# Kernel tuning notes

Measured on AMD Instinct MI355X. Metric: run time of the kernel, lower is better.

The kernel has to match this reference:

```python
import jax, jax.numpy as jnp
import numpy as np

B, T, S = 2, 1024, 2048            # batch, query len, cache size
D, N, KH, H = 4096, 32, 8, 128     # emb_dim, q heads, kv heads, head_dim
ROPE_THETA = 1000000
EPS = 1e-6
K_MASK = jnp.finfo(jnp.bfloat16).min


def _rms_norm(x, scale):
    dtype = x.dtype
    rms = jnp.sqrt(jnp.mean(x.astype(jnp.float32) ** 2, axis=-1, keepdims=True) + EPS)
    return (scale * x / rms).astype(dtype)


def _rope_sincos(positions, head_dim):
    fraction = jnp.arange(0, head_dim, 2, dtype=jnp.float32) / head_dim
    inv_freq = 1.0 / (ROPE_THETA ** fraction)
    sinusoid = jnp.einsum('BT,k->BTk', positions.astype(jnp.float32), inv_freq,
                          precision=jax.lax.Precision.HIGHEST)
    return jnp.sin(sinusoid), jnp.cos(sinusoid)


def _apply_rope(x, sin, cos):
    half = x.shape[-1] // 2
    x1, x2 = x[..., :half], x[..., half:]
    sin, cos = sin[:, :, None, :], cos[:, :, None, :]
    return jnp.concatenate([x1 * cos - x2 * sin, x2 * cos + x1 * sin], axis=-1).astype(x.dtype)


def setup_inputs() -> dict:
    key = jax.random.key(0)
    ks = jax.random.split(key, 8)
    std = 0.01  # nnx.initializers.normal() default stddev
    return {
        'x': jax.random.normal(ks[0], (B, T, D), dtype=jnp.float32),
        'wq': jax.random.normal(ks[1], (D, N, H), dtype=jnp.float32) * std,
        'wk': jax.random.normal(ks[2], (D, KH, H), dtype=jnp.float32) * std,
        'wv': jax.random.normal(ks[3], (D, KH, H), dtype=jnp.float32) * std,
        'wo': jax.random.normal(ks[4], (N, H, D), dtype=jnp.float32) * std,
        'q_scale': jnp.ones((H,), dtype=jnp.float32),
        'k_scale': jnp.ones((H,), dtype=jnp.float32),
        'k_cache': jnp.zeros((B, S, KH, H), dtype=jnp.float32),
        'v_cache': jnp.zeros((B, S, KH, H), dtype=jnp.float32),
        'segment_ids': jnp.ones((B, T), dtype=jnp.int32),
        'num_right_pads': 0,
    }


def reference(x, wq, wk, wv, wo, q_scale, k_scale, k_cache, v_cache, segment_ids, num_right_pads):
    b, t, _ = x.shape
    s = k_cache.shape[1]
    n, kh, h = wq.shape[1], wk.shape[1], wq.shape[2]
    cur_ind = 0  # empty cache (prefill)

    q = _rms_norm(jnp.einsum('BTD,DNH->BTNH', x, wq), q_scale)      # [B,T,N,H]
    key = _rms_norm(jnp.einsum('BSD,DKH->BSKH', x, wk), k_scale)    # [B,T,K,H]
    val = jnp.einsum('BSD,DKH->BSKH', x, wv)                         # [B,T,K,H]

    # start_ind < 0 initially -> count left pads from segment_ids
    start = jnp.sum(jnp.cumsum(segment_ids != 0, axis=-1) == 0, -1).astype(jnp.int32)
    first = jnp.argmax(segment_ids, axis=1)
    pos = jnp.where(segment_ids != 0, jnp.arange(t, dtype=jnp.int32) - first[:, None], 2 ** 30)
    position_ids = pos + cur_ind

    sin, cos = _rope_sincos(position_ids, h)
    q = _apply_rope(q, sin, cos)
    key = _apply_rope(key, sin, cos)

    k_cache = jax.lax.dynamic_update_slice(k_cache, key, (0, cur_ind, 0, 0))
    v_cache = jax.lax.dynamic_update_slice(v_cache, val, (0, cur_ind, 0, 0))

    g = n // kh
    qr = q.reshape(b, t, kh, g, h)
    logits = jnp.einsum('BTHGD,BSHD->BHGTS', qr, k_cache) * (h ** -0.5)

    q_pos = cur_ind + jnp.arange(t, dtype=jnp.int32)[None, :] - start[:, None]
    ts = jnp.arange(s, dtype=jnp.int32)
    kv_seg = ((ts[None, :] >= start[:, None]) & (ts[None, :] < cur_ind + t)).astype(segment_ids.dtype)
    k_pos = ts[None, :] - start[:, None]
    causal = k_pos[:, None, :] <= q_pos[:, :, None]                  # [B,T,S]
    seg_mask = kv_seg[:, None, :] == segment_ids[:, :, None]        # [B,T,S]
    mask = causal & seg_mask

    logits = jnp.where(mask[:, None, None, :, :], logits, K_MASK)
    w = jax.nn.softmax(logits.astype(jnp.float32), axis=-1).astype(logits.dtype)
    qkv = jnp.einsum('BHGTS,BSHD->BTHGD', w, v_cache).reshape(b, t, n, h)
    return jnp.einsum('BTNH,NHD->BTD', qkv, wo)
```

## Files before the change

kernel.cpp:

```cpp
#include <hip/hip_runtime.h>

constexpr int Bc  = 2;
constexpr int Tc  = 1024;
constexpr int Dc  = 4096;
constexpr int NHc = 32;
constexpr int KHc = 8;
constexpr int Hc  = 128;

typedef __bf16 bf16;
typedef bf16  bf16x4  __attribute__((ext_vector_type(4)));
typedef bf16  bf16x8  __attribute__((ext_vector_type(8)));
typedef float floatx4 __attribute__((ext_vector_type(4)));

#define MFMA16(a, b, c) __builtin_amdgcn_mfma_f32_16x16x32_bf16((a), (b), (c), 0, 0, 0)

__device__ __forceinline__ void gload_lds16(const bf16* g, bf16* l) {
    __builtin_amdgcn_global_load_lds(
        (const __attribute__((address_space(1))) void*)g,
        (__attribute__((address_space(3))) void*)l, 16, 0, 0);
}

__global__ void seg_scan(const int* __restrict__ seg, int* __restrict__ start) {
    int b = threadIdx.x;
    if (b >= Bc) return;
    int f = 0;
    for (int t = 0; t < Tc; ++t) {
        if (seg[b * Tc + t] != 0) { f = t; break; }
    }
    start[b] = f;
}

__global__ __launch_bounds__(256) void cvt_f32_bf16(const float* __restrict__ in,
                                                    bf16* __restrict__ out) {
    const size_t i = ((size_t)blockIdx.x * 256 + threadIdx.x) * 8;
    float4 f0 = *(const float4*)(in + i);
    float4 f1 = *(const float4*)(in + i + 4);
    bf16x8 v;
    v[0] = (bf16)f0.x; v[1] = (bf16)f0.y; v[2] = (bf16)f0.z; v[3] = (bf16)f0.w;
    v[4] = (bf16)f1.x; v[5] = (bf16)f1.y; v[6] = (bf16)f1.z; v[7] = (bf16)f1.w;
    *(bf16x8*)(out + i) = v;
}

__global__ __launch_bounds__(256) void transpose_cvt(const float* __restrict__ in,
                                                     bf16* __restrict__ out,
                                                     int R, int C) {
    __shared__ float tile[64][65];
    const int c0 = blockIdx.x * 64, r0 = blockIdx.y * 64;
    const int tx = threadIdx.x & 15, ty = threadIdx.x >> 4;
#pragma unroll
    for (int i = 0; i < 4; ++i) {
        float4 f = *(const float4*)&in[(size_t)(r0 + ty * 4 + i) * C + c0 + tx * 4];
        tile[ty * 4 + i][tx * 4 + 0] = f.x;
        tile[ty * 4 + i][tx * 4 + 1] = f.y;
        tile[ty * 4 + i][tx * 4 + 2] = f.z;
        tile[ty * 4 + i][tx * 4 + 3] = f.w;
    }
    __syncthreads();
#pragma unroll
    for (int i = 0; i < 4; ++i) {
        const int cc = ty * 4 + i;
        bf16x4 v;
        v[0] = (bf16)tile[tx * 4 + 0][cc];
        v[1] = (bf16)tile[tx * 4 + 1][cc];
        v[2] = (bf16)tile[tx * 4 + 2][cc];
        v[3] = (bf16)tile[tx * 4 + 3][cc];
        *(bf16x4*)&out[(size_t)(c0 + cc) * R + r0 + tx * 4] = v;
    }
}

__global__ __launch_bounds__(256) void v_transpose(const bf16* __restrict__ src,
                                                   bf16* __restrict__ dst,
                                                   int srcstride) {
    __shared__ bf16 tl[32][136];
    const int bk = blockIdx.y;
    const int b = bk / KHc, kh = bk % KHc;
    const int t0 = blockIdx.x * 32;
    const int tid = threadIdx.x;
    {
        const int j = tid >> 3;
        const int c = tid & 7;
        const bf16* p = src + (size_t)(b * Tc + t0 + j) * srcstride + kh * Hc + c * 16;
        *(bf16x8*)&tl[j][c * 16]     = *(const bf16x8*)p;
        *(bf16x8*)&tl[j][c * 16 + 8] = *(const bf16x8*)(p + 8);
    }
    __syncthreads();
    {
        const int d = tid >> 1;
        const int toff = (tid & 1) * 16;
        bf16x8 v0, v1;
#pragma unroll
        for (int k = 0; k < 8; ++k) v0[k] = tl[toff + k][d];
#pragma unroll
        for (int k = 0; k < 8; ++k) v1[k] = tl[toff + 8 + k][d];
        bf16* o = dst + ((size_t)bk * Hc + d) * Tc + t0 + toff;
        *(bf16x8*)o       = v0;
        *(bf16x8*)(o + 8) = v1;
    }
}

template <typename OT>
__global__ __launch_bounds__(256) void gemm128(const bf16* __restrict__ A,
                                               const bf16* __restrict__ Bt,
                                               OT* __restrict__ C,
                                               int M, int K, int N) {
    __shared__ alignas(16) bf16 As[128 * 32];
    __shared__ alignas(16) bf16 Bs[128 * 32];
    const int m0 = blockIdx.y * 128, n0 = blockIdx.x * 128;
    const int tid = threadIdx.x;
    const int w = tid >> 6, L = tid & 63, quad = L >> 4, lid = L & 15;
    const int wm = (w & 1) * 64, wn = (w >> 1) * 64;

    const int srow = w * 32 + (L >> 2);
    const int chk  = (L & 3) ^ ((L >> 3) & 3);
    const bf16* gA = A  + (size_t)(m0 + srow) * K + chk * 8;
    const bf16* gB = Bt + (size_t)(n0 + srow) * K + chk * 8;
    bf16* lA0 = &As[(w * 32) * 32];
    bf16* lA1 = &As[(w * 32 + 16) * 32];
    bf16* lB0 = &Bs[(w * 32) * 32];
    bf16* lB1 = &Bs[(w * 32 + 16) * 32];

    const bf16* ap[4]; const bf16* bp[4];
#pragma unroll
    for (int i = 0; i < 4; ++i) {
        const int ra = wm + i * 16 + lid;
        ap[i] = &As[ra * 32 + (quad ^ ((ra >> 1) & 3)) * 8];
        const int rb = wn + i * 16 + lid;
        bp[i] = &Bs[rb * 32 + (quad ^ ((rb >> 1) & 3)) * 8];
    }

    floatx4 acc[4][4] = {};

    for (int k0 = 0; k0 < K; k0 += 32) {
        __syncthreads();
        gload_lds16(gA + k0,                  lA0);
        gload_lds16(gA + (size_t)16 * K + k0, lA1);
        gload_lds16(gB + k0,                  lB0);
        gload_lds16(gB + (size_t)16 * K + k0, lB1);
        __syncthreads();

        bf16x8 af[4], bfr[4];
#pragma unroll
        for (int i = 0; i < 4; ++i) af[i]  = *(const bf16x8*)ap[i];
#pragma unroll
        for (int j = 0; j < 4; ++j) bfr[j] = *(const bf16x8*)bp[j];
#pragma unroll
        for (int i = 0; i < 4; ++i)
#pragma unroll
            for (int j = 0; j < 4; ++j)
                acc[i][j] = MFMA16(af[i], bfr[j], acc[i][j]);
    }

#pragma unroll
    for (int i = 0; i < 4; ++i) {
#pragma unroll
        for (int r = 0; r < 4; ++r) {
            const size_t row = (size_t)(m0 + wm + i * 16 + quad * 4 + r);
#pragma unroll
            for (int j = 0; j < 4; ++j)
                C[row * N + (n0 + wn + j * 16 + lid)] = (OT)acc[i][j][r];
        }
    }
}

template <typename OT>
__global__ __launch_bounds__(512, 2) void gemm_ring256(const bf16* __restrict__ A,
                                                       const bf16* __restrict__ Bt,
                                                       OT* __restrict__ C,
                                                       int M, int K, int N) {
    __shared__ alignas(16) bf16 ring[4][16384];
    const int m0 = blockIdx.y * 256, n0 = blockIdx.x * 256;
    const int tid = threadIdx.x;
    const int w = tid >> 6, L = tid & 63, quad = L >> 4, lid = L & 15;
    const int wr = w >> 2, wc = w & 3;

    const int srow = tid >> 2;
    const int schk = ((tid & 3) ^ ((tid >> 3) & 3)) * 8;
    const bf16* gA0 = A  + (size_t)(m0 + srow) * K + schk;
    const bf16* gA1 = A  + (size_t)(m0 + 128 + srow) * K + schk;
    const bf16* gB0 = Bt + (size_t)(n0 + srow) * K + schk;
    const bf16* gB1 = Bt + (size_t)(n0 + 128 + srow) * K + schk;
    const int ldsA0 = (w * 16) * 32;
    const int ldsA1 = (128 + w * 16) * 32;
    const int ldsB0 = 8192 + (w * 16) * 32;
    const int ldsB1 = 8192 + (128 + w * 16) * 32;

    int offA[8], offB[4];
#pragma unroll
    for (int m = 0; m < 8; ++m) {
        const int row = wr * 128 + m * 16 + lid;
        offA[m] = row * 32 + ((quad ^ ((row >> 1) & 3)) * 8);
    }
#pragma unroll
    for (int n = 0; n < 4; ++n) {
        const int row = wc * 64 + n * 16 + lid;
        offB[n] = 8192 + row * 32 + ((quad ^ ((row >> 1) & 3)) * 8);
    }

    const int NT = K >> 5;

    auto stage = [&](int kt) {
        bf16* sb = ring[kt & 3];
        const size_t ko = (size_t)kt << 5;
        gload_lds16(gA0 + ko, sb + ldsA0);
        gload_lds16(gA1 + ko, sb + ldsA1);
        gload_lds16(gB0 + ko, sb + ldsB0);
        gload_lds16(gB1 + ko, sb + ldsB1);
    };

    stage(0); stage(1); stage(2);
    asm volatile("s_waitcnt vmcnt(8)" ::: "memory");
    __builtin_amdgcn_s_barrier();
    __builtin_amdgcn_sched_barrier(0);

    floatx4 acc[8][4] = {};

    for (int t = 0; t < NT; ++t) {
        int ts = t + 3; if (ts >= NT) ts -= NT;
        stage(ts);

        const bf16* sb = ring[t & 3];
        bf16x8 af[8], bfr[4];
#pragma unroll
        for (int m = 0; m < 8; ++m) af[m]  = *(const bf16x8*)(sb + offA[m]);
#pragma unroll
        for (int n = 0; n < 4; ++n) bfr[n] = *(const bf16x8*)(sb + offB[n]);

        __builtin_amdgcn_s_setprio(1);
#pragma unroll
        for (int m = 0; m < 8; ++m)
#pragma unroll
            for (int n = 0; n < 4; ++n)
                acc[m][n] = MFMA16(af[m], bfr[n], acc[m][n]);
        __builtin_amdgcn_s_setprio(0);

        asm volatile("s_waitcnt vmcnt(8)" ::: "memory");
        __builtin_amdgcn_s_barrier();
        __builtin_amdgcn_sched_barrier(0);
    }

    asm volatile("s_waitcnt vmcnt(0)" ::: "memory");

#pragma unroll
    for (int m = 0; m < 8; ++m) {
#pragma unroll
        for (int r = 0; r < 4; ++r) {
            const size_t row = (size_t)(m0 + wr * 128 + m * 16 + quad * 4 + r);
#pragma unroll
            for (int n = 0; n < 4; ++n)
                C[row * N + (n0 + wc * 64 + n * 16 + lid)] = (OT)acc[m][n][r];
        }
    }
}

__global__ __launch_bounds__(256) void rms_rope(bf16* __restrict__ buf,
                                                const float* __restrict__ scale,
                                                const int* __restrict__ start,
                                                int nheads, int rowstride) {
    const int gid = blockIdx.x * 4 + (threadIdx.x >> 6);
    const int L   = threadIdx.x & 63;
    const int h   = gid % nheads;
    const int t   = (gid / nheads) % Tc;
    const int b   = gid / (nheads * Tc);
    bf16* p = buf + (size_t)(b * Tc + t) * rowstride + h * Hc;

    float x1 = (float)p[L], x2 = (float)p[L + 64];
    float ss = x1 * x1 + x2 * x2;
#pragma unroll
    for (int off = 1; off < 64; off <<= 1) ss += __shfl_xor(ss, off);
    const float inv = 1.f / sqrtf(ss * (1.0f / 128.0f) + 1e-6f);
    const float y1 = scale[L] * x1 * inv;
    const float y2 = scale[L + 64] * x2 * inv;

    const int   pos = t - start[b];
    const float fr  = (float)L * (1.0f / 64.0f);
    const float invf = exp2f(-19.9315686f * fr);
    const float ang = (float)pos * invf;
    float sn, cs;
    sincosf(ang, &sn, &cs);

    p[L]      = (bf16)(y1 * cs - y2 * sn);
    p[L + 64] = (bf16)(y2 * cs + y1 * sn);
}

__global__ __launch_bounds__(256) void attn_kernel(const bf16* __restrict__ q,
                                                   const bf16* __restrict__ k,
                                                   const bf16* __restrict__ vt,
                                                   bf16* __restrict__ outp,
                                                   const int* __restrict__ start,
                                                   int qstride, int kstride) {
    __shared__ alignas(16) bf16 Ks[32 * 128];
    __shared__ alignas(16) bf16 VT[128 * 32];
    __shared__ alignas(16) bf16 pS[4][16][40];

    const int tblk = blockIdx.x, n = blockIdx.y, b = blockIdx.z;
    const int kh   = n >> 2;
    const int tid  = threadIdx.x, w = tid >> 6, L = tid & 63;
    const int quad = L >> 4, lid = L & 15;
    const int t0   = tblk * 64 + w * 16;
    const int st   = start[b];

    const bf16* qrow = q + (size_t)(b * Tc + t0 + lid) * qstride + n * Hc;
    bf16x8 aqf[4];
#pragma unroll
    for (int c = 0; c < 4; ++c) aqf[c] = *(const bf16x8*)(qrow + c * 32 + quad * 8);

    const int kr0 = w * 8 + (L >> 4);
    const int kr1 = kr0 + 4;
    const bf16* gK0 = k + (size_t)(b * Tc + kr0) * kstride + kh * Hc
                        + (((L & 15) ^ (kr0 & 15)) * 8);
    const bf16* gK1 = k + (size_t)(b * Tc + kr1) * kstride + kh * Hc
                        + (((L & 15) ^ (kr1 & 15)) * 8);
    bf16* lK0 = &Ks[(w * 8) * 128];
    bf16* lK1 = &Ks[(w * 8 + 4) * 128];

    const int vd0 = (w * 2) * 16 + (L >> 2);
    const int vd1 = vd0 + 16;
    const bf16* vbase = vt + (size_t)((b * KHc + kh) * Hc) * Tc;
    const bf16* gV0 = vbase + (size_t)vd0 * Tc + (((L & 3) ^ (vd0 & 3) ^ ((vd0 >> 2) & 3)) * 8);
    const bf16* gV1 = vbase + (size_t)vd1 * Tc + (((L & 3) ^ (vd1 & 3) ^ ((vd1 >> 2) & 3)) * 8);
    bf16* lV0 = &VT[(w * 2) * 512];
    bf16* lV1 = &VT[(w * 2 + 1) * 512];

    const bf16* kf[4][2];
#pragma unroll
    for (int c = 0; c < 4; ++c) {
        kf[c][0] = &Ks[lid * 128        + (((c * 4 + quad) ^ lid) * 8)];
        kf[c][1] = &Ks[(16 + lid) * 128 + (((c * 4 + quad) ^ lid) * 8)];
    }
    const int vpos = (quad ^ (lid & 3) ^ ((lid >> 2) & 3)) * 8;
    const bf16* vf[8];
#pragma unroll
    for (int cg = 0; cg < 8; ++cg) vf[cg] = &VT[(cg * 16 + lid) * 32 + vpos];

    floatx4 oacc[8] = {};
    float lsum[4] = {0.f, 0.f, 0.f, 0.f};
    const int sEnd = tblk * 64 + 64;

    for (int s0 = 0; s0 < sEnd; s0 += 32) {
        __syncthreads();
        gload_lds16(gK0 + (size_t)s0 * kstride, lK0);
        gload_lds16(gK1 + (size_t)s0 * kstride, lK1);
        gload_lds16(gV0 + s0, lV0);
        gload_lds16(gV1 + s0, lV1);
        __syncthreads();

        floatx4 sc0 = {0.f, 0.f, 0.f, 0.f}, sc1 = {0.f, 0.f, 0.f, 0.f};
#pragma unroll
        for (int c = 0; c < 4; ++c) {
            sc0 = MFMA16(aqf[c], *(const bf16x8*)kf[c][0], sc0);
            sc1 = MFMA16(aqf[c], *(const bf16x8*)kf[c][1], sc1);
        }

#pragma unroll
        for (int r = 0; r < 4; ++r) {
            const int tq  = t0 + quad * 4 + r;
            const int sk0 = s0 + lid, sk1 = s0 + 16 + lid;
            const float p0 = (sk0 <= tq && sk0 >= st)
                               ? __expf(sc0[r] * 0.08838834764831845f - 16.f) : 0.f;
            const float p1 = (sk1 <= tq && sk1 >= st)
                               ? __expf(sc1[r] * 0.08838834764831845f - 16.f) : 0.f;
            lsum[r] += p0 + p1;
            pS[w][quad * 4 + r][lid]      = (bf16)p0;
            pS[w][quad * 4 + r][16 + lid] = (bf16)p1;
        }
        asm volatile("s_waitcnt lgkmcnt(0)" ::: "memory");

        bf16x8 pa = *(const bf16x8*)&pS[w][lid][quad * 8];
#pragma unroll
        for (int cg = 0; cg < 8; ++cg)
            oacc[cg] = MFMA16(pa, *(const bf16x8*)vf[cg], oacc[cg]);
    }

#pragma unroll
    for (int r = 0; r < 4; ++r) {
        lsum[r] += __shfl_xor(lsum[r], 1);
        lsum[r] += __shfl_xor(lsum[r], 2);
        lsum[r] += __shfl_xor(lsum[r], 4);
        lsum[r] += __shfl_xor(lsum[r], 8);
    }

#pragma unroll
    for (int cg = 0; cg < 8; ++cg) {
#pragma unroll
        for (int r = 0; r < 4; ++r) {
            const int t = t0 + quad * 4 + r;
            outp[((size_t)(b * Tc + t) * NHc + n) * Hc + cg * 16 + lid] =
                (bf16)(oacc[cg][r] / lsum[r]);
        }
    }
}

extern "C" void kernel_launch(void* const* d_in, const int* in_sizes, int n_in,
                              void* d_out, int out_size, void* d_ws, size_t ws_size,
                              hipStream_t stream) {
    const float* x       = (const float*)d_in[0];
    const float* wq      = (const float*)d_in[1];
    const float* wk      = (const float*)d_in[2];
    const float* wv      = (const float*)d_in[3];
    const float* wo      = (const float*)d_in[4];
    const float* q_scale = (const float*)d_in[5];
    const float* k_scale = (const float*)d_in[6];
    const int*   seg     = (const int*)d_in[9];
    float*       out     = (float*)d_out;

    char* ws = (char*)d_ws;
    bf16* wcomb = (bf16*)(ws);
    bf16* vtb   = (bf16*)(ws + (32ull << 20));
    bf16* qkvb  = (bf16*)(ws + (48ull << 20));
    bf16* xb    = (bf16*)(ws + (72ull << 20));
    bf16* ab    = xb;
    int*  stb   = (int*) (ws + (88ull << 20));

    seg_scan<<<1, 64, 0, stream>>>(seg, stb);

    cvt_f32_bf16<<<(Bc * Tc * Dc) / (256 * 8), 256, 0, stream>>>(x, xb);

    transpose_cvt<<<dim3(64, 64), 256, 0, stream>>>(wq, wcomb, Dc, NHc * Hc);
    transpose_cvt<<<dim3(16, 64), 256, 0, stream>>>(wk, wcomb + (size_t)4096 * Dc, Dc, KHc * Hc);
    transpose_cvt<<<dim3(16, 64), 256, 0, stream>>>(wv, wcomb + (size_t)5120 * Dc, Dc, KHc * Hc);

    gemm_ring256<bf16><<<dim3(24, 8), 512, 0, stream>>>(xb, wcomb, qkvb,
                                                        Bc * Tc, Dc, 6144);

    rms_rope<<<(Bc * Tc * NHc) / 4, 256, 0, stream>>>(qkvb, q_scale, stb, NHc, 6144);
    rms_rope<<<(Bc * Tc * KHc) / 4, 256, 0, stream>>>(qkvb + 4096, k_scale, stb, KHc, 6144);

    v_transpose<<<dim3(Tc / 32, Bc * KHc), 256, 0, stream>>>(qkvb + 5120, vtb, 6144);

    transpose_cvt<<<dim3(64, 64), 256, 0, stream>>>(wo, wcomb, NHc * Hc, Dc);

    attn_kernel<<<dim3(Tc / 64, NHc, Bc), 256, 0, stream>>>(
        qkvb, qkvb + 4096, vtb, ab, stb, 6144, 6144);

    gemm128<float><<<dim3(32, 16), 256, 0, stream>>>(ab, wcomb, out,
                                                     Bc * Tc, NHc * Hc, Dc);
}
```

Before: 530.3 us.

## Split GEMM main loop into two half-phases interleaving LDS reads, global prefetch and MFMA

Result: no change. 534.8 us (+0.8%).

```diff
diff --git a/kernel.cpp b/kernel.cpp
--- a/kernel.cpp
+++ b/kernel.cpp
@@ -198,16 +198,20 @@
 
     const int NT = K >> 5;
 
-    auto stage = [&](int kt) {
+    auto stageA = [&](int kt) {
         bf16* sb = ring[kt & 3];
         const size_t ko = (size_t)kt << 5;
         gload_lds16(gA0 + ko, sb + ldsA0);
         gload_lds16(gA1 + ko, sb + ldsA1);
+    };
+    auto stageB = [&](int kt) {
+        bf16* sb = ring[kt & 3];
+        const size_t ko = (size_t)kt << 5;
         gload_lds16(gB0 + ko, sb + ldsB0);
         gload_lds16(gB1 + ko, sb + ldsB1);
     };
 
-    stage(0); stage(1); stage(2);
+    stageA(0); stageB(0); stageA(1); stageB(1); stageA(2); stageB(2);
     asm volatile("s_waitcnt vmcnt(8)" ::: "memory");
     __builtin_amdgcn_s_barrier();
     __builtin_amdgcn_sched_barrier(0);
@@ -216,21 +220,42 @@
 
     for (int t = 0; t < NT; ++t) {
         int ts = t + 3; if (ts >= NT) ts -= NT;
-        stage(ts);
-
         const bf16* sb = ring[t & 3];
-        bf16x8 af[8], bfr[4];
-#pragma unroll
-        for (int m = 0; m < 8; ++m) af[m]  = *(const bf16x8*)(sb + offA[m]);
+
+        bf16x8 af0[4], bfr[4];
+#pragma unroll
+        for (int m = 0; m < 4; ++m) af0[m] = *(const bf16x8*)(sb + offA[m]);
 #pragma unroll
         for (int n = 0; n < 4; ++n) bfr[n] = *(const bf16x8*)(sb + offB[n]);
-
+        stageA(ts);
+
+        __builtin_amdgcn_s_barrier();
+        asm volatile("s_waitcnt lgkmcnt(0)" ::: "memory");
+        __builtin_amdgcn_sched_barrier(0);
         __builtin_amdgcn_s_setprio(1);
 #pragma unroll
-        for (int m = 0; m < 8; ++m)
+        for (int m = 0; m < 4; ++m)
 #pragma unroll
             for (int n = 0; n < 4; ++n)
-                acc[m][n] = MFMA16(af[m], bfr[n], acc[m][n]);
+                acc[m][n] = MFMA16(af0[m], bfr[n], acc[m][n]);
+        __builtin_amdgcn_s_setprio(0);
+        __builtin_amdgcn_s_barrier();
+        __builtin_amdgcn_sched_barrier(0);
+
+        bf16x8 af1[4];
+#pragma unroll
+        for (int m = 0; m < 4; ++m) af1[m] = *(const bf16x8*)(sb + offA[4 + m]);
+        stageB(ts);
+
+        __builtin_amdgcn_s_barrier();
+        asm volatile("s_waitcnt lgkmcnt(0)" ::: "memory");
+        __builtin_amdgcn_sched_barrier(0);
+        __builtin_amdgcn_s_setprio(1);
+#pragma unroll
+        for (int m = 0; m < 4; ++m)
+#pragma unroll
+            for (int n = 0; n < 4; ++n)
+                acc[4 + m][n] = MFMA16(af1[m], bfr[n], acc[4 + m][n]);
         __builtin_amdgcn_s_setprio(0);
 
         asm volatile("s_waitcnt vmcnt(8)" ::: "memory");
```
